# Performance work log

Hardware: AMD Instinct MI355X
Metric: run time of the kernel (lower is better)

## Reference

```python
import jax, jax.numpy as jnp
import numpy as np

B, S, T, H, V = 32, 64, 64, 512, 32000


def setup_inputs() -> dict:
    key = jax.random.key(0)
    ks = jax.random.split(key, 16)
    sc = 1.0 / np.sqrt(H)
    return {
        "encoder_outputs": jax.random.normal(ks[0], (B, S, H), jnp.float32),
        "encoder_hidden": jax.random.normal(ks[1], (1, B, H), jnp.float32),
        "target_tensor": jax.random.randint(ks[2], (B, T), 0, V),
        "max_len": T,
        "emb": jax.random.normal(ks[3], (V, H), jnp.float32) * 0.02,
        "Wa_w": jax.random.normal(ks[4], (H, H), jnp.float32) * sc,
        "Wa_b": jnp.zeros((H,), jnp.float32),
        "Ua_w": jax.random.normal(ks[5], (H, H), jnp.float32) * sc,
        "Ua_b": jnp.zeros((H,), jnp.float32),
        "Va_w": jax.random.normal(ks[6], (1, H), jnp.float32) * sc,
        "Va_b": jnp.zeros((1,), jnp.float32),
        "W_ih": jax.random.normal(ks[7], (3 * H, 2 * H), jnp.float32) * sc,
        "W_hh": jax.random.normal(ks[8], (3 * H, H), jnp.float32) * sc,
        "b_ih": jnp.zeros((3 * H,), jnp.float32),
        "b_hh": jnp.zeros((3 * H,), jnp.float32),
        "out_w": jax.random.normal(ks[9], (V, H), jnp.float32) * sc,
        "out_b": jnp.zeros((V,), jnp.float32),
    }


def reference(encoder_outputs, encoder_hidden, target_tensor, max_len,
              emb, Wa_w, Wa_b, Ua_w, Ua_b, Va_w, Va_b,
              W_ih, W_hh, b_ih, b_hh, out_w, out_b):
    # Teacher-forcing decode; dropout in eval mode (identity).
    keys = encoder_outputs                      # [B,S,H]
    Ua_keys = keys @ Ua_w.T + Ua_b              # precompute Ua(keys): same math each step
    bsz = keys.shape[0]
    # token fed at step 0 is SOS (=0), then target_tensor[:, i-1]
    tokens = jnp.concatenate(
        [jnp.zeros((bsz, 1), target_tensor.dtype), target_tensor[:, : max_len - 1]], axis=1
    )  # [B,T]

    def step(h, tok):                            # h: [B,H], tok: [B]
        e = emb[tok]                             # [B,H] embedding gather
        q = h @ Wa_w.T + Wa_b                    # Wa(query)
        s = jnp.tanh(q[:, None, :] + Ua_keys)    # [B,S,H]
        scores = (s @ Va_w.T + Va_b)[..., 0]     # [B,S]
        w = jax.nn.softmax(scores, axis=-1)      # [B,S]
        ctx = jnp.einsum('bs,bsh->bh', w, keys)  # [B,H]
        x = jnp.concatenate([e, ctx], axis=-1)   # [B,2H]
        gi = x @ W_ih.T + b_ih                   # [B,3H]
        gh = h @ W_hh.T + b_hh                   # [B,3H]
        ir, iz, inn = jnp.split(gi, 3, axis=-1)
        hr, hz, hn = jnp.split(gh, 3, axis=-1)
        r = jax.nn.sigmoid(ir + hr)
        z = jax.nn.sigmoid(iz + hz)
        n = jnp.tanh(inn + r * hn)
        h_new = (1.0 - z) * n + z * h            # GRU cell (PyTorch convention)
        logits = h_new @ out_w.T + out_b         # [B,V]
        return h_new, (logits, w)

    h0 = encoder_hidden[0]                       # [B,H]
    hT, (logits, attn) = jax.lax.scan(step, h0, jnp.swapaxes(tokens, 0, 1))
    logits = jnp.swapaxes(logits, 0, 1)          # [B,T,V]
    decoder_outputs = jax.nn.log_softmax(logits, axis=-1)
    attentions = jnp.swapaxes(attn, 0, 1)        # [B,T,S]
    return decoder_outputs, hT[None], attentions
```

## Files before the change

### kernel.cpp

```cpp
#include <hip/hip_runtime.h>
#include <hip/hip_bf16.h>
#include <hip/hip_fp16.h>
#include <math.h>

constexpr int B = 32, S = 64, T = 64, H = 512, V = 32000;
constexpr int G3 = 3 * H;
constexpr int BT = B * T;

constexpr size_t UAK_OFF    = 0;
constexpr size_t GIE_OFF    = 1048576;
constexpr size_t KWTH_OFF   = 4194304;
constexpr size_t WA2T_OFF   = 5767168;
constexpr size_t WHH2T_OFF  = 5898240;
constexpr size_t ROWIDX_OFF = 6291456;
constexpr size_t SCPT_OFF   = 6293504;
constexpr size_t FLG_OFF    = 7342080;
constexpr size_t OWBF_OFF   = 0;
constexpr size_t HALL_OFF   = 8192000;
constexpr size_t STATS_OFF  = 8192000;
constexpr size_t HBF_OFF    = 9256960;
constexpr size_t KEYSH_OFF  = 10000000;
constexpr size_t GEH_OFF    = 10524288;
constexpr size_t UAWH_OFF   = 11048576;
constexpr size_t WLOH_OFF   = 11179648;
constexpr size_t WCTXH_OFF  = 11572864;

typedef __attribute__((ext_vector_type(8))) short bf16x8;
typedef __attribute__((ext_vector_type(4))) float f32x4;
typedef _Float16 f16x8 __attribute__((ext_vector_type(8)));
typedef _Float16 h2v __attribute__((ext_vector_type(2)));

__device__ __forceinline__ float fast_tanh(float x) {
  float ax = fabsf(x);
  float e = __expf(-2.f * ax);
  float r = (1.f - e) / (1.f + e);
  return x < 0.f ? -r : r;
}
__device__ __forceinline__ float fast_sig(float x) {
  return 1.f / (1.f + __expf(-x));
}
__device__ __forceinline__ unsigned pack_h2(float a, float b) {
  __half2 h = __floats2half2_rn(a, b);
  return *(unsigned*)&h;
}
__device__ __forceinline__ ushort f2h(float v) {
  __half h = __float2half(v);
  return *(ushort*)&h;
}
__device__ __forceinline__ void unp2(unsigned v, float* d) {
  __half2 h = *(__half2*)&v;
  d[0] = __low2float(h); d[1] = __high2float(h);
}
__device__ __forceinline__ float dot2acc(unsigned w, unsigned h, float c) {
  return __builtin_amdgcn_fdot2(__builtin_bit_cast(h2v, w),
                                __builtin_bit_cast(h2v, h), c, false);
}
__device__ __forceinline__ int load_coh_i32(const int* p) {
  int v;
  asm volatile("global_load_dword %0, %1, off sc0 sc1\n\ts_waitcnt vmcnt(0)"
               : "=v"(v) : "v"(p) : "memory");
  return v;
}
__device__ __forceinline__ void store_coh_f32x4(float* p, f32x4 v) {
  asm volatile("global_store_dwordx4 %0, %1, off sc0 sc1" :: "v"(p), "v"(v) : "memory");
}

__global__ void k_init(const float* __restrict__ eh, const int* __restrict__ tgt,
                       float* __restrict__ ws) {
  int i = blockIdx.x * 256 + threadIdx.x;
  if (i < B * H) ws[HALL_OFF + i] = eh[i];
  if (i < BT) {
    int b = i / T, t = i % T;
    ((int*)(ws + ROWIDX_OFF))[i] = (t == 0) ? 0 : tgt[b * T + t - 1];
  }
  if (i < T * 64) ((int*)(ws + FLG_OFF))[i] = 0;
}

__global__ void k_conv_f16(const float* __restrict__ in, int ld, int coloff,
                           const int* __restrict__ rowidx, ushort* __restrict__ out,
                           int rows) {
  int i4 = (blockIdx.x * 256 + threadIdx.x) * 4;
  if (i4 < rows * 512) {
    int row = i4 >> 9, k = i4 & 511;
    int ar = rowidx ? rowidx[row] : row;
    float4 v = *(const float4*)&in[(size_t)ar * ld + coloff + k];
    ushort4 o;
    o.x = f2h(v.x); o.y = f2h(v.y); o.z = f2h(v.z); o.w = f2h(v.w);
    *(ushort4*)&out[i4] = o;
  }
}

__global__ void k_pack_t(const float* __restrict__ in, unsigned* __restrict__ out, int R) {
  int i = blockIdx.x * 256 + threadIdx.x;
  if (i < R * 256) {
    int r = i >> 8, kk = i & 255;
    float2 v = *(const float2*)&in[(size_t)r * 512 + 2 * kk];
    out[(size_t)kk * R + r] = pack_h2(v.x, v.y);
  }
}

__global__ void k_conv_outw(const float* __restrict__ w, ushort* __restrict__ o, int n4) {
  int i = blockIdx.x * blockDim.x + threadIdx.x;
  if (i < n4) {
    float4 v = *(const float4*)&w[(size_t)i * 4];
    ushort4 u;
    __hip_bfloat16 h0 = __float2bfloat16(v.x); u.x = *(ushort*)&h0;
    __hip_bfloat16 h1 = __float2bfloat16(v.y); u.y = *(ushort*)&h1;
    __hip_bfloat16 h2 = __float2bfloat16(v.z); u.z = *(ushort*)&h2;
    __hip_bfloat16 h3 = __float2bfloat16(v.w); u.w = *(ushort*)&h3;
    *(ushort4*)&o[(size_t)i * 4] = u;
  }
}

__global__ __launch_bounds__(256) void k_mfma128(
    const ushort* __restrict__ Ah, const ushort* __restrict__ Bh,
    const float* __restrict__ bias, float* __restrict__ C, int ldc) {
  __shared__ __align__(16) ushort As[128 * 32];
  __shared__ __align__(16) ushort Bs[128 * 32];
  int bm = blockIdx.y, bn = blockIdx.x;
  int tid = threadIdx.x;
  int lane = tid & 63, wv = tid >> 6;
  int wm = wv >> 1, wn = wv & 1;
  int kc = lane >> 4, rl = lane & 15;
  f32x4 acc[4][4] = {};
  int c0 = wv * 128 + lane, c1 = c0 + 64;
  const ushort* ga0 = Ah + (size_t)(bm * 128 + (c0 >> 2)) * 512 + (c0 & 3) * 8;
  const ushort* ga1 = Ah + (size_t)(bm * 128 + (c1 >> 2)) * 512 + (c1 & 3) * 8;
  const ushort* gb0 = Bh + (size_t)(bn * 128 + (c0 >> 2)) * 512 + (c0 & 3) * 8;
  const ushort* gb1 = Bh + (size_t)(bn * 128 + (c1 >> 2)) * 512 + (c1 & 3) * 8;
  for (int k0 = 0; k0 < 512; k0 += 32) {
    __syncthreads();
    __builtin_amdgcn_global_load_lds(
        (const __attribute__((address_space(1))) void*)(ga0 + k0),
        (__attribute__((address_space(3))) void*)((char*)As + wv * 2048), 16, 0, 0);
    __builtin_amdgcn_global_load_lds(
        (const __attribute__((address_space(1))) void*)(ga1 + k0),
        (__attribute__((address_space(3))) void*)((char*)As + wv * 2048 + 1024), 16, 0, 0);
    __builtin_amdgcn_global_load_lds(
        (const __attribute__((address_space(1))) void*)(gb0 + k0),
        (__attribute__((address_space(3))) void*)((char*)Bs + wv * 2048), 16, 0, 0);
    __builtin_amdgcn_global_load_lds(
        (const __attribute__((address_space(1))) void*)(gb1 + k0),
        (__attribute__((address_space(3))) void*)((char*)Bs + wv * 2048 + 1024), 16, 0, 0);
    __syncthreads();
    f16x8 af[4], bfv[4];
#pragma unroll
    for (int f = 0; f < 4; f++) {
      af[f] = *(const f16x8*)&As[(wm * 64 + f * 16 + rl) * 32 + kc * 8];
      bfv[f] = *(const f16x8*)&Bs[(wn * 64 + f * 16 + rl) * 32 + kc * 8];
    }
#pragma unroll
    for (int i = 0; i < 4; i++)
#pragma unroll
      for (int j = 0; j < 4; j++)
        acc[i][j] = __builtin_amdgcn_mfma_f32_16x16x32_f16(af[i], bfv[j], acc[i][j], 0, 0, 0);
  }
  int cl = lane & 15, rg = lane >> 4;
#pragma unroll
  for (int i = 0; i < 4; i++) {
    int m = bm * 128 + wm * 64 + i * 16 + rg * 4;
#pragma unroll
    for (int j = 0; j < 4; j++) {
      int n = bn * 128 + wn * 64 + j * 16 + cl;
      float bv = bias[n];
#pragma unroll
      for (int r = 0; r < 4; r++)
        C[(size_t)(m + r) * ldc + n] = acc[i][j][r] + bv;
    }
  }
}

__global__ __launch_bounds__(256) void k_mfma_kwt(
    const ushort* __restrict__ Wctxh, const ushort* __restrict__ keysh,
    ushort* __restrict__ KWTh) {
  __shared__ __align__(16) ushort As[128 * 32];
  __shared__ __align__(16) ushort Bs[64 * 32];
  int bm = blockIdx.x, b = blockIdx.y;
  int tid = threadIdx.x;
  int lane = tid & 63, wv = tid >> 6;
  int kc = lane >> 4, rl = lane & 15;
  f32x4 acc[2][4] = {};
  int c0 = tid, c2 = tid + 256;
  const ushort* ga0 = Wctxh + (size_t)(bm * 128 + (c0 >> 2)) * 512 + (c0 & 3) * 8;
  const ushort* ga1 = Wctxh + (size_t)(bm * 128 + (c2 >> 2)) * 512 + (c2 & 3) * 8;
  const ushort* gb0 = keysh + (size_t)(b * 64 + (c0 >> 2)) * 512 + (c0 & 3) * 8;
  for (int k0 = 0; k0 < 512; k0 += 32) {
    __syncthreads();
    __builtin_amdgcn_global_load_lds(
        (const __attribute__((address_space(1))) void*)(ga0 + k0),
        (__attribute__((address_space(3))) void*)((char*)As + wv * 1024), 16, 0, 0);
    __builtin_amdgcn_global_load_lds(
        (const __attribute__((address_space(1))) void*)(ga1 + k0),
        (__attribute__((address_space(3))) void*)((char*)As + 4096 + wv * 1024), 16, 0, 0);
    __builtin_amdgcn_global_load_lds(
        (const __attribute__((address_space(1))) void*)(gb0 + k0),
        (__attribute__((address_space(3))) void*)((char*)Bs + wv * 1024), 16, 0, 0);
    __syncthreads();
    f16x8 af[2], bfv[4];
#pragma unroll
    for (int f = 0; f < 2; f++)
      af[f] = *(const f16x8*)&As[(wv * 32 + f * 16 + rl) * 32 + kc * 8];
#pragma unroll
    for (int j = 0; j < 4; j++)
      bfv[j] = *(const f16x8*)&Bs[(j * 16 + rl) * 32 + kc * 8];
#pragma unroll
    for (int i = 0; i < 2; i++)
#pragma unroll
      for (int j = 0; j < 4; j++)
        acc[i][j] = __builtin_amdgcn_mfma_f32_16x16x32_f16(af[i], bfv[j], acc[i][j], 0, 0, 0);
  }
  int cl = lane & 15, rg = lane >> 4;
#pragma unroll
  for (int i = 0; i < 2; i++) {
    int m = bm * 128 + wv * 32 + i * 16 + rg * 4;
#pragma unroll
    for (int j = 0; j < 4; j++) {
      int n = j * 16 + cl;
#pragma unroll
      for (int r = 0; r < 4; r++)
        KWTh[((size_t)b * G3 + m + r) * 64 + n] = f2h(acc[i][j][r]);
    }
  }
}

__global__ __launch_bounds__(256) void k_recur(
    const float* __restrict__ Wa_b, const float* __restrict__ Va_w,
    const float* __restrict__ Va_b, const float* __restrict__ b_hh,
    const unsigned* __restrict__ WA2T, const unsigned* __restrict__ WHH2T,
    float* __restrict__ ws, float* __restrict__ attn_out) {
  const int w = blockIdx.x;
  const int tid = threadIdx.x;
  const int b = w & 31, cb = w >> 5;
  const int j0 = cb * 64;
  int* flg = (int*)(ws + FLG_OFF);
  __hip_bfloat16* HBF = (__hip_bfloat16*)(ws + HBF_OFF);
  const float* GIE = ws + GIE_OFF;
  float* SCPT = ws + SCPT_OFF;
  const ushort* KWTh = (const ushort*)(ws + KWTH_OFF);

  __shared__ float sKWT[192][68];
  __shared__ float sUAK[64][68];
  __shared__ float sh[512];
  __shared__ unsigned sH2[256];
  __shared__ float sq[64];
  __shared__ float qp[64][5];
  __shared__ float spp[64][5];
  __shared__ float sps[64];
  __shared__ float scg[8][64];
  __shared__ float swt[64];
  __shared__ float sga[4][64];
  __shared__ float shn[64];
  __shared__ float sVa[64], sWab[64], sBhh[192];

#pragma unroll
  for (int g = 0; g < 3; g++) {
    int jl = tid >> 2, part = tid & 3;
    const ushort* src = KWTh + ((size_t)b * G3 + g * 512 + j0 + jl) * 64 + part * 16;
    float* dst = &sKWT[g * 64 + jl][part * 16];
    uint4 u0 = *(const uint4*)src;
    uint4 u1 = *(const uint4*)(src + 8);
    unp2(u0.x, dst); unp2(u0.y, dst + 2); unp2(u0.z, dst + 4); unp2(u0.w, dst + 6);
    unp2(u1.x, dst + 8); unp2(u1.y, dst + 10); unp2(u1.z, dst + 12); unp2(u1.w, dst + 14);
  }
  {
    int s = tid >> 2, part = tid & 3;
    const float* src = ws + UAK_OFF + ((size_t)(b * 64 + s)) * 512 + j0 + part * 16;
    float* dst = &sUAK[s][part * 16];
#pragma unroll
    for (int i = 0; i < 16; i += 4) *(float4*)&dst[i] = *(const float4*)&src[i];
  }
  if (tid < 64) { sVa[tid] = Va_w[j0 + tid]; sWab[tid] = Wa_b[j0 + tid]; }
  if (tid < 192) sBhh[tid] = b_hh[(tid >> 6) * 512 + j0 + (tid & 63)];
  const float va_b = Va_b[0];
  __syncthreads();

  for (int t = 0; t < T; ++t) {
    if (t > 0) {
      if (tid == 0)
        while (load_coh_i32(&flg[(t - 1) * 64 + b * 2]) != 8) __builtin_amdgcn_s_sleep(1);
    }
    __syncthreads();
    const float* hcur = ws + HALL_OFF + (size_t)t * B * H + b * H;
    sh[tid] = hcur[tid];
    sh[tid + 256] = hcur[tid + 256];
    float gival = 0.f;
    if (tid < 192)
      gival = GIE[((size_t)b * T + t) * G3 + (tid >> 6) * 512 + j0 + (tid & 63)];
    __syncthreads();
    if (tid < 256) sH2[tid] = pack_h2(sh[2 * tid], sh[2 * tid + 1]);
    __syncthreads();

    {
      int jq = tid & 63, kp = tid >> 6;
      const unsigned* wp = WA2T + (size_t)(kp * 64) * 512 + j0 + jq;
      float acc = 0.f;
#pragma unroll 8
      for (int kk = 0; kk < 64; kk++)
        acc = dot2acc(wp[(size_t)kk * 512], sH2[kp * 64 + kk], acc);
      qp[jq][kp] = acc;
    }
    __syncthreads();
    if (tid < 64)
      sq[tid] = qp[tid][0] + qp[tid][1] + qp[tid][2] + qp[tid][3] + sWab[tid];
    __syncthreads();
    {
      int s = tid >> 2, jc = tid & 3;
      float accs = 0.f;
#pragma unroll
      for (int i = 0; i < 16; i++) {
        int j = jc * 16 + i;
        accs += sVa[j] * fast_tanh(sq[j] + sUAK[s][j]);
      }
      spp[s][jc] = accs;
    }
    __syncthreads();
    if (tid < 64) {
      float v = spp[tid][0] + spp[tid][1] + spp[tid][2] + spp[tid][3];
      if (cb == 0) v += va_b;
      sps[tid] = v;
    }
    __syncthreads();
    if (tid < 16)
      store_coh_f32x4(SCPT + (((size_t)t * B + b) * 8 + cb) * 64 + tid * 4,
                      *(f32x4*)&sps[tid * 4]);
    if (tid == 0) {
      asm volatile("s_waitcnt vmcnt(0)" ::: "memory");
      __hip_atomic_fetch_add(&flg[t * 64 + b * 2 + 1], 1,
                             __ATOMIC_RELAXED, __HIP_MEMORY_SCOPE_AGENT);
    }

    float gh = 0.f;
    if (tid < 192) {
      int gate = tid >> 6, lane = tid & 63;
      const unsigned* wp = WHH2T + gate * 512 + j0 + lane;
      float g0 = 0.f, g1 = 0.f;
#pragma unroll 8
      for (int kk = 0; kk < 256; kk += 2) {
        g0 = dot2acc(wp[(size_t)kk * 1536], sH2[kk], g0);
        g1 = dot2acc(wp[(size_t)(kk + 1) * 1536], sH2[kk + 1], g1);
      }
      gh = g0 + g1 + sBhh[tid];
    }
    if (tid == 0)
      while (load_coh_i32(&flg[t * 64 + b * 2 + 1]) != 8) __builtin_amdgcn_s_sleep(1);
    __syncthreads();
    if (tid < 128) {
      f32x4 v = *(const f32x4*)&SCPT[((size_t)t * B + b) * 512 + tid * 4];
      *(f32x4*)&scg[tid >> 4][(tid & 15) * 4] = v;
    }
    __syncthreads();
    if (tid < 64) {
      float v = scg[0][tid] + scg[1][tid] + scg[2][tid] + scg[3][tid]
              + scg[4][tid] + scg[5][tid] + scg[6][tid] + scg[7][tid];
      float m = v;
      for (int o = 32; o; o >>= 1) m = fmaxf(m, __shfl_xor(m, o, 64));
      float e = __expf(v - m);
      float su = e;
      for (int o = 32; o; o >>= 1) su += __shfl_xor(su, o, 64);
      float wt = e / su;
      swt[tid] = wt;
      if (cb == 0) attn_out[((size_t)b * T + t) * S + tid] = wt;
    }
    __syncthreads();
    if (tid < 192) {
      int gate = tid >> 6, lane = tid & 63;
      float gic = 0.f;
#pragma unroll
      for (int s4 = 0; s4 < 64; s4 += 4) {
        float4 k4 = *(const float4*)&sKWT[tid][s4];
        gic += k4.x * swt[s4] + k4.y * swt[s4 + 1] + k4.z * swt[s4 + 2] + k4.w * swt[s4 + 3];
      }
      float gi = gival + gic;
      if (gate == 0) sga[0][lane] = gi + gh;
      else if (gate == 1) sga[1][lane] = gi + gh;
      else { sga[2][lane] = gi; sga[3][lane] = gh; }
    }
    __syncthreads();
    if (tid < 64) {
      float r = fast_sig(sga[0][tid]);
      float z = fast_sig(sga[1][tid]);
      float n = fast_tanh(sga[2][tid] + r * sga[3][tid]);
      float hold = sh[j0 + tid];
      float hn = (1.f - z) * n + z * hold;
      shn[tid] = hn;
      HBF[((size_t)b * T + t) * H + j0 + tid] = __float2bfloat16(hn);
    }
    __syncthreads();
    if (tid < 16)
      store_coh_f32x4(ws + HALL_OFF + (size_t)(t + 1) * B * H + b * H + j0 + tid * 4,
                      *(f32x4*)&shn[tid * 4]);
    if (tid == 0) {
      asm volatile("s_waitcnt vmcnt(0)" ::: "memory");
      __hip_atomic_fetch_add(&flg[t * 64 + b * 2], 1,
                             __ATOMIC_RELAXED, __HIP_MEMORY_SCOPE_AGENT);
    }
  }
}

__global__ __launch_bounds__(256) void k_outgemm(
    const __hip_bfloat16* __restrict__ Abf, const __hip_bfloat16* __restrict__ Bbf,
    const float* __restrict__ bias, float* __restrict__ Cmat,
    float* __restrict__ stats) {
  __shared__ __align__(16) short As[128 * 32];
  __shared__ __align__(16) short Bs[128 * 32];
  __shared__ float sredM[2][128];
  __shared__ float sredS[2][128];
  int bm = blockIdx.y, bn = blockIdx.x;
  int tid = threadIdx.x;
  int lane = tid & 63, wv = tid >> 6;
  int wm = wv >> 1, wn = wv & 1;
  int kc = lane >> 4, rl = lane & 15;
  f32x4 acc[4][4] = {};
  int c0 = wv * 128 + lane, c1 = c0 + 64;
  const __hip_bfloat16* ga0 = Abf + (size_t)(bm * 128 + (c0 >> 2)) * 512 + (c0 & 3) * 8;
  const __hip_bfloat16* ga1 = Abf + (size_t)(bm * 128 + (c1 >> 2)) * 512 + (c1 & 3) * 8;
  const __hip_bfloat16* gb0 = Bbf + (size_t)(bn * 128 + (c0 >> 2)) * 512 + (c0 & 3) * 8;
  const __hip_bfloat16* gb1 = Bbf + (size_t)(bn * 128 + (c1 >> 2)) * 512 + (c1 & 3) * 8;
  for (int k0 = 0; k0 < 512; k0 += 32) {
    __syncthreads();
    __builtin_amdgcn_global_load_lds(
        (const __attribute__((address_space(1))) void*)(ga0 + k0),
        (__attribute__((address_space(3))) void*)((char*)As + wv * 2048), 16, 0, 0);
    __builtin_amdgcn_global_load_lds(
        (const __attribute__((address_space(1))) void*)(ga1 + k0),
        (__attribute__((address_space(3))) void*)((char*)As + wv * 2048 + 1024), 16, 0, 0);
    __builtin_amdgcn_global_load_lds(
        (const __attribute__((address_space(1))) void*)(gb0 + k0),
        (__attribute__((address_space(3))) void*)((char*)Bs + wv * 2048), 16, 0, 0);
    __builtin_amdgcn_global_load_lds(
        (const __attribute__((address_space(1))) void*)(gb1 + k0),
        (__attribute__((address_space(3))) void*)((char*)Bs + wv * 2048 + 1024), 16, 0, 0);
    __syncthreads();
    bf16x8 af[4], bfv[4];
#pragma unroll
    for (int f = 0; f < 4; f++) {
      af[f] = *(const bf16x8*)&As[(wm * 64 + f * 16 + rl) * 32 + kc * 8];
      bfv[f] = *(const bf16x8*)&Bs[(wn * 64 + f * 16 + rl) * 32 + kc * 8];
    }
#pragma unroll
    for (int i = 0; i < 4; i++)
#pragma unroll
      for (int j = 0; j < 4; j++)
        acc[i][j] = __builtin_amdgcn_mfma_f32_16x16x32_bf16(af[i], bfv[j], acc[i][j], 0, 0, 0);
  }
  int cl = lane & 15, rg = lane >> 4;
  float bv[4];
#pragma unroll
  for (int j = 0; j < 4; j++) bv[j] = bias[bn * 128 + wn * 64 + j * 16 + cl];
  float vmax[4][4];
#pragma unroll
  for (int i = 0; i < 4; i++) {
    int m = bm * 128 + wm * 64 + i * 16 + rg * 4;
#pragma unroll
    for (int r = 0; r < 4; r++) vmax[i][r] = -1e30f;
#pragma unroll
    for (int j = 0; j < 4; j++) {
      int n = bn * 128 + wn * 64 + j * 16 + cl;
#pragma unroll
      for (int r = 0; r < 4; r++) {
        float val = acc[i][j][r] + bv[j];
        Cmat[(size_t)(m + r) * V + n] = val;
        vmax[i][r] = fmaxf(vmax[i][r], val);
      }
    }
  }
#pragma unroll
  for (int o = 1; o < 16; o <<= 1)
#pragma unroll
    for (int i = 0; i < 4; i++)
#pragma unroll
      for (int r = 0; r < 4; r++)
        vmax[i][r] = fmaxf(vmax[i][r], __shfl_xor(vmax[i][r], o, 64));
  float vsum[4][4] = {};
#pragma unroll
  for (int i = 0; i < 4; i++)
#pragma unroll
    for (int j = 0; j < 4; j++)
#pragma unroll
      for (int r = 0; r < 4; r++)
        vsum[i][r] += __expf(acc[i][j][r] + bv[j] - vmax[i][r]);
#pragma unroll
  for (int o = 1; o < 16; o <<= 1)
#pragma unroll
    for (int i = 0; i < 4; i++)
#pragma unroll
      for (int r = 0; r < 4; r++)
        vsum[i][r] += __shfl_xor(vsum[i][r], o, 64);
  if (cl == 0) {
#pragma unroll
    for (int i = 0; i < 4; i++)
#pragma unroll
      for (int r = 0; r < 4; r++) {
        int rowl = wm * 64 + i * 16 + rg * 4 + r;
        sredM[wn][rowl] = vmax[i][r];
        sredS[wn][rowl] = vsum[i][r];
      }
  }
  __syncthreads();
  if (tid < 128) {
    float m0 = sredM[0][tid], m1 = sredM[1][tid];
    float M = fmaxf(m0, m1);
    float Sv = sredS[0][tid] * __expf(m0 - M) + sredS[1][tid] * __expf(m1 - M);
    float* st = stats + (size_t)(bm * 128 + tid) * 512 + bn * 2;
    st[0] = M; st[1] = Sv;
  }
}

__global__ __launch_bounds__(256) void k_lsm_final(float* __restrict__ Cmat,
                                                   const float* __restrict__ stats) {
  int row = blockIdx.x;
  int tid = threadIdx.x;
  __shared__ float sM[4], sS[4];
  float m = -1e30f, s = 0.f;
  if (tid < 250) {
    float2 v = *(const float2*)&stats[(size_t)row * 512 + tid * 2];
    m = v.x; s = v.y;
  }
  for (int o = 32; o; o >>= 1) {
    float om = __shfl_xor(m, o, 64), os = __shfl_xor(s, o, 64);
    float nm = fmaxf(m, om);
    s = s * __expf(m - nm) + os * __expf(om - nm);
    m = nm;
  }
  if ((tid & 63) == 0) { sM[tid >> 6] = m; sS[tid >> 6] = s; }
  __syncthreads();
  float M = fmaxf(fmaxf(sM[0], sM[1]), fmaxf(sM[2], sM[3]));
  float Ssum = sS[0] * __expf(sM[0] - M) + sS[1] * __expf(sM[1] - M)
             + sS[2] * __expf(sM[2] - M) + sS[3] * __expf(sM[3] - M);
  float lse = M + __logf(Ssum);
  float* p = Cmat + (size_t)row * V;
  for (int i = tid * 4; i < V; i += 1024) {
    float4 v = *(const float4*)&p[i];
    v.x -= lse; v.y -= lse; v.z -= lse; v.w -= lse;
    *(float4*)&p[i] = v;
  }
}

__global__ void k_copy_ht(const float* __restrict__ hsrc, float* __restrict__ o) {
  int i = blockIdx.x * 256 + threadIdx.x;
  if (i < B * H) o[i] = hsrc[i];
}

extern "C" void kernel_launch(void* const* d_in, const int* in_sizes, int n_in,
                              void* d_out, int out_size, void* d_ws, size_t ws_size,
                              hipStream_t stream) {
  (void)in_sizes; (void)n_in; (void)out_size; (void)ws_size;
  const float* keys = (const float*)d_in[0];
  const float* ehid = (const float*)d_in[1];
  const int* tgt    = (const int*)d_in[2];
  const float* emb  = (const float*)d_in[4];
  const float* Wa_w = (const float*)d_in[5];
  const float* Wa_b = (const float*)d_in[6];
  const float* Ua_w = (const float*)d_in[7];
  const float* Ua_b = (const float*)d_in[8];
  const float* Va_w = (const float*)d_in[9];
  const float* Va_b = (const float*)d_in[10];
  const float* W_ih = (const float*)d_in[11];
  const float* W_hh = (const float*)d_in[12];
  const float* b_ih = (const float*)d_in[13];
  const float* b_hh = (const float*)d_in[14];
  const float* out_w = (const float*)d_in[15];
  const float* out_b = (const float*)d_in[16];
  float* ws = (float*)d_ws;
  float* out = (float*)d_out;
  float* logits = out;
  float* ht_out = out + (size_t)B * T * V;
  float* attn_out = ht_out + (size_t)B * H;

  hipLaunchKernelGGL(k_init, dim3(64), dim3(256), 0, stream, ehid, tgt, ws);
  hipLaunchKernelGGL(k_conv_f16, dim3(1024), dim3(256), 0, stream,
                     keys, 512, 0, (const int*)nullptr, (ushort*)(ws + KEYSH_OFF), 2048);
  hipLaunchKernelGGL(k_conv_f16, dim3(1024), dim3(256), 0, stream,
                     emb, 512, 0, (const int*)(ws + ROWIDX_OFF), (ushort*)(ws + GEH_OFF), 2048);
  hipLaunchKernelGGL(k_conv_f16, dim3(256), dim3(256), 0, stream,
                     Ua_w, 512, 0, (const int*)nullptr, (ushort*)(ws + UAWH_OFF), 512);
  hipLaunchKernelGGL(k_conv_f16, dim3(768), dim3(256), 0, stream,
                     W_ih, 1024, 0, (const int*)nullptr, (ushort*)(ws + WLOH_OFF), 1536);
  hipLaunchKernelGGL(k_conv_f16, dim3(768), dim3(256), 0, stream,
                     W_ih, 1024, 512, (const int*)nullptr, (ushort*)(ws + WCTXH_OFF), 1536);
  hipLaunchKernelGGL(k_pack_t, dim3(512), dim3(256), 0, stream,
                     Wa_w, (unsigned*)(ws + WA2T_OFF), 512);
  hipLaunchKernelGGL(k_pack_t, dim3(1536), dim3(256), 0, stream,
                     W_hh, (unsigned*)(ws + WHH2T_OFF), 1536);
  hipLaunchKernelGGL(k_mfma128, dim3(4, 16), dim3(256), 0, stream,
                     (const ushort*)(ws + KEYSH_OFF), (const ushort*)(ws + UAWH_OFF),
                     Ua_b, ws + UAK_OFF, 512);
  hipLaunchKernelGGL(k_mfma128, dim3(12, 16), dim3(256), 0, stream,
                     (const ushort*)(ws + GEH_OFF), (const ushort*)(ws + WLOH_OFF),
                     b_ih, ws + GIE_OFF, G3);
  hipLaunchKernelGGL(k_mfma_kwt, dim3(12, 32), dim3(256), 0, stream,
                     (const ushort*)(ws + WCTXH_OFF), (const ushort*)(ws + KEYSH_OFF),
                     (ushort*)(ws + KWTH_OFF));
  hipLaunchKernelGGL(k_recur, dim3(256), dim3(256), 0, stream,
                     Wa_b, Va_w, Va_b, b_hh,
                     (const unsigned*)(ws + WA2T_OFF), (const unsigned*)(ws + WHH2T_OFF),
                     ws, attn_out);
  hipLaunchKernelGGL(k_copy_ht, dim3(64), dim3(256), 0, stream,
                     ws + HALL_OFF + (size_t)T * B * H, ht_out);
  hipLaunchKernelGGL(k_conv_outw, dim3((V * H / 4 + 255) / 256), dim3(256), 0, stream,
                     out_w, (ushort*)(ws + OWBF_OFF), V * H / 4);
  hipLaunchKernelGGL(k_outgemm, dim3(250, 16), dim3(256), 0, stream,
                     (const __hip_bfloat16*)(ws + HBF_OFF),
                     (const __hip_bfloat16*)(ws + OWBF_OFF), out_b, logits,
                     ws + STATS_OFF);
  hipLaunchKernelGGL(k_lsm_final, dim3(BT), dim3(256), 0, stream,
                     logits, ws + STATS_OFF);
}
```

Baseline: 1.013 ms.

## Replace atomic counters with per-block flag slots and merge prep kernels

Inter-block sync in the recurrent kernel now uses one flag slot per column block, polled with two coherent 16-byte loads, instead of atomic counters polled with sleeps. It also drops several shared-memory staging steps and barriers by storing h and score partials directly with coherent scalar stores. Eight small preprocessing launches become one multi-role k_prep kernel, and the final hidden state is written inside the recurrence, removing the copy kernel. This targets per-step sync latency and launch overhead, at the cost of more flag memory and busy-spinning without sleep.

```diff
diff --git a/kernel.cpp b/kernel.cpp
--- a/kernel.cpp
+++ b/kernel.cpp
@@ -12,9 +12,8 @@
 constexpr size_t KWTH_OFF   = 4194304;
 constexpr size_t WA2T_OFF   = 5767168;
 constexpr size_t WHH2T_OFF  = 5898240;
-constexpr size_t ROWIDX_OFF = 6291456;
-constexpr size_t SCPT_OFF   = 6293504;
-constexpr size_t FLG_OFF    = 7342080;
+constexpr size_t SCPT_OFF   = 6291456;
+constexpr size_t FLG_OFF    = 7340032;
 constexpr size_t OWBF_OFF   = 0;
 constexpr size_t HALL_OFF   = 8192000;
 constexpr size_t STATS_OFF  = 8192000;
@@ -27,6 +26,7 @@
 
 typedef __attribute__((ext_vector_type(8))) short bf16x8;
 typedef __attribute__((ext_vector_type(4))) float f32x4;
+typedef __attribute__((ext_vector_type(4))) int i32x4;
 typedef _Float16 f16x8 __attribute__((ext_vector_type(8)));
 typedef _Float16 h2v __attribute__((ext_vector_type(2)));
 
@@ -55,47 +55,84 @@
   return __builtin_amdgcn_fdot2(__builtin_bit_cast(h2v, w),
                                 __builtin_bit_cast(h2v, h), c, false);
 }
-__device__ __forceinline__ int load_coh_i32(const int* p) {
-  int v;
-  asm volatile("global_load_dword %0, %1, off sc0 sc1\n\ts_waitcnt vmcnt(0)"
-               : "=v"(v) : "v"(p) : "memory");
-  return v;
-}
-__device__ __forceinline__ void store_coh_f32x4(float* p, f32x4 v) {
-  asm volatile("global_store_dwordx4 %0, %1, off sc0 sc1" :: "v"(p), "v"(v) : "memory");
-}
-
-__global__ void k_init(const float* __restrict__ eh, const int* __restrict__ tgt,
+__device__ __forceinline__ int poll8(const int* p) {
+  i32x4 a, b;
+  asm volatile("global_load_dwordx4 %0, %2, off sc0 sc1\n\t"
+               "global_load_dwordx4 %1, %3, off sc0 sc1\n\t"
+               "s_waitcnt vmcnt(0)"
+               : "=v"(a), "=v"(b) : "v"(p), "v"(p + 4) : "memory");
+  return a.x & a.y & a.z & a.w & b.x & b.y & b.z & b.w;
+}
+__device__ __forceinline__ void store_coh_i32(int* p, int v) {
+  asm volatile("global_store_dword %0, %1, off sc0 sc1" :: "v"(p), "v"(v) : "memory");
+}
+__device__ __forceinline__ void store_coh_f32(float* p, float v) {
+  asm volatile("global_store_dword %0, %1, off sc0 sc1" :: "v"(p), "v"(v) : "memory");
+}
+
+__global__ void k_prep(const float* __restrict__ eh, const int* __restrict__ tgt,
+                       const float* __restrict__ keys, const float* __restrict__ emb,
+                       const float* __restrict__ Ua_w, const float* __restrict__ W_ih,
+                       const float* __restrict__ Wa_w, const float* __restrict__ W_hh,
                        float* __restrict__ ws) {
-  int i = blockIdx.x * 256 + threadIdx.x;
-  if (i < B * H) ws[HALL_OFF + i] = eh[i];
-  if (i < BT) {
-    int b = i / T, t = i % T;
-    ((int*)(ws + ROWIDX_OFF))[i] = (t == 0) ? 0 : tgt[b * T + t - 1];
-  }
-  if (i < T * 64) ((int*)(ws + FLG_OFF))[i] = 0;
-}
-
-__global__ void k_conv_f16(const float* __restrict__ in, int ld, int coloff,
-                           const int* __restrict__ rowidx, ushort* __restrict__ out,
-                           int rows) {
-  int i4 = (blockIdx.x * 256 + threadIdx.x) * 4;
-  if (i4 < rows * 512) {
+  int blk = blockIdx.x, tid = threadIdx.x;
+  if (blk < 256) {
+    int i = blk * 256 + tid;
+    ((int*)(ws + FLG_OFF))[i] = 0;
+    if (i < B * H) ws[HALL_OFF + i] = eh[i];
+    return;
+  }
+  if (blk < 1280) {
+    int i4 = ((blk - 256) * 256 + tid) * 4;
+    float4 v = *(const float4*)&keys[i4];
+    ushort4 o; o.x = f2h(v.x); o.y = f2h(v.y); o.z = f2h(v.z); o.w = f2h(v.w);
+    *(ushort4*)&((ushort*)(ws + KEYSH_OFF))[i4] = o;
+    return;
+  }
+  if (blk < 2304) {
+    int i4 = ((blk - 1280) * 256 + tid) * 4;
     int row = i4 >> 9, k = i4 & 511;
-    int ar = rowidx ? rowidx[row] : row;
-    float4 v = *(const float4*)&in[(size_t)ar * ld + coloff + k];
-    ushort4 o;
-    o.x = f2h(v.x); o.y = f2h(v.y); o.z = f2h(v.z); o.w = f2h(v.w);
-    *(ushort4*)&out[i4] = o;
-  }
-}
-
-__global__ void k_pack_t(const float* __restrict__ in, unsigned* __restrict__ out, int R) {
-  int i = blockIdx.x * 256 + threadIdx.x;
-  if (i < R * 256) {
+    int tok = (row & 63) ? tgt[row - 1] : 0;
+    float4 v = *(const float4*)&emb[(size_t)tok * 512 + k];
+    ushort4 o; o.x = f2h(v.x); o.y = f2h(v.y); o.z = f2h(v.z); o.w = f2h(v.w);
+    *(ushort4*)&((ushort*)(ws + GEH_OFF))[i4] = o;
+    return;
+  }
+  if (blk < 2560) {
+    int i4 = ((blk - 2304) * 256 + tid) * 4;
+    float4 v = *(const float4*)&Ua_w[i4];
+    ushort4 o; o.x = f2h(v.x); o.y = f2h(v.y); o.z = f2h(v.z); o.w = f2h(v.w);
+    *(ushort4*)&((ushort*)(ws + UAWH_OFF))[i4] = o;
+    return;
+  }
+  if (blk < 3328) {
+    int i4 = ((blk - 2560) * 256 + tid) * 4;
+    int row = i4 >> 9, k = i4 & 511;
+    float4 v = *(const float4*)&W_ih[(size_t)row * 1024 + k];
+    ushort4 o; o.x = f2h(v.x); o.y = f2h(v.y); o.z = f2h(v.z); o.w = f2h(v.w);
+    *(ushort4*)&((ushort*)(ws + WLOH_OFF))[i4] = o;
+    return;
+  }
+  if (blk < 4096) {
+    int i4 = ((blk - 3328) * 256 + tid) * 4;
+    int row = i4 >> 9, k = i4 & 511;
+    float4 v = *(const float4*)&W_ih[(size_t)row * 1024 + 512 + k];
+    ushort4 o; o.x = f2h(v.x); o.y = f2h(v.y); o.z = f2h(v.z); o.w = f2h(v.w);
+    *(ushort4*)&((ushort*)(ws + WCTXH_OFF))[i4] = o;
+    return;
+  }
+  if (blk < 4608) {
+    int i = (blk - 4096) * 256 + tid;
     int r = i >> 8, kk = i & 255;
-    float2 v = *(const float2*)&in[(size_t)r * 512 + 2 * kk];
-    out[(size_t)kk * R + r] = pack_h2(v.x, v.y);
+    float2 v = *(const float2*)&Wa_w[(size_t)r * 512 + 2 * kk];
+    ((unsigned*)(ws + WA2T_OFF))[(size_t)kk * 512 + r] = pack_h2(v.x, v.y);
+    return;
+  }
+  {
+    int i = (blk - 4608) * 256 + tid;
+    int r = i >> 8, kk = i & 255;
+    float2 v = *(const float2*)&W_hh[(size_t)r * 512 + 2 * kk];
+    ((unsigned*)(ws + WHH2T_OFF))[(size_t)kk * 1536 + r] = pack_h2(v.x, v.y);
   }
 }
 
@@ -227,7 +264,7 @@
     const float* __restrict__ Wa_b, const float* __restrict__ Va_w,
     const float* __restrict__ Va_b, const float* __restrict__ b_hh,
     const unsigned* __restrict__ WA2T, const unsigned* __restrict__ WHH2T,
-    float* __restrict__ ws, float* __restrict__ attn_out) {
+    float* __restrict__ ws, float* __restrict__ attn_out, float* __restrict__ ht_out) {
   const int w = blockIdx.x;
   const int tid = threadIdx.x;
   const int b = w & 31, cb = w >> 5;
@@ -240,16 +277,12 @@
 
   __shared__ float sKWT[192][68];
   __shared__ float sUAK[64][68];
-  __shared__ float sh[512];
   __shared__ unsigned sH2[256];
   __shared__ float sq[64];
   __shared__ float qp[64][5];
   __shared__ float spp[64][5];
-  __shared__ float sps[64];
-  __shared__ float scg[8][64];
   __shared__ float swt[64];
   __shared__ float sga[4][64];
-  __shared__ float shn[64];
   __shared__ float sVa[64], sWab[64], sBhh[192];
 
 #pragma unroll
@@ -275,19 +308,21 @@
   __syncthreads();
 
   for (int t = 0; t < T; ++t) {
-    if (t > 0) {
-      if (tid == 0)
-        while (load_coh_i32(&flg[(t - 1) * 64 + b * 2]) != 8) __builtin_amdgcn_s_sleep(1);
-    }
-    __syncthreads();
     const float* hcur = ws + HALL_OFF + (size_t)t * B * H + b * H;
-    sh[tid] = hcur[tid];
-    sh[tid + 256] = hcur[tid + 256];
     float gival = 0.f;
     if (tid < 192)
       gival = GIE[((size_t)b * T + t) * G3 + (tid >> 6) * 512 + j0 + (tid & 63)];
-    __syncthreads();
-    if (tid < 256) sH2[tid] = pack_h2(sh[2 * tid], sh[2 * tid + 1]);
+    if (t > 0) {
+      if (tid == 0) {
+        const int* fb = flg + (size_t)(t - 1) * 1024 + b * 32;
+        while (!poll8(fb)) {}
+      }
+    }
+    __syncthreads();
+    {
+      float2 h2 = *(const float2*)&hcur[2 * tid];
+      sH2[tid] = pack_h2(h2.x, h2.y);
+    }
     __syncthreads();
 
     {
@@ -317,16 +352,11 @@
     if (tid < 64) {
       float v = spp[tid][0] + spp[tid][1] + spp[tid][2] + spp[tid][3];
       if (cb == 0) v += va_b;
-      sps[tid] = v;
-    }
-    __syncthreads();
-    if (tid < 16)
-      store_coh_f32x4(SCPT + (((size_t)t * B + b) * 8 + cb) * 64 + tid * 4,
-                      *(f32x4*)&sps[tid * 4]);
+      store_coh_f32(SCPT + (((size_t)t * B + b) * 8 + cb) * 64 + tid, v);
+    }
     if (tid == 0) {
       asm volatile("s_waitcnt vmcnt(0)" ::: "memory");
-      __hip_atomic_fetch_add(&flg[t * 64 + b * 2 + 1], 1,
-                             __ATOMIC_RELAXED, __HIP_MEMORY_SCOPE_AGENT);
+      store_coh_i32(flg + (size_t)t * 1024 + b * 32 + 8 + cb, 1);
     }
 
     float gh = 0.f;
@@ -341,17 +371,15 @@
       }
       gh = g0 + g1 + sBhh[tid];
     }
-    if (tid == 0)
-      while (load_coh_i32(&flg[t * 64 + b * 2 + 1]) != 8) __builtin_amdgcn_s_sleep(1);
-    __syncthreads();
-    if (tid < 128) {
-      f32x4 v = *(const f32x4*)&SCPT[((size_t)t * B + b) * 512 + tid * 4];
-      *(f32x4*)&scg[tid >> 4][(tid & 15) * 4] = v;
+    if (tid == 0) {
+      const int* fs = flg + (size_t)t * 1024 + b * 32 + 8;
+      while (!poll8(fs)) {}
     }
     __syncthreads();
     if (tid < 64) {
-      float v = scg[0][tid] + scg[1][tid] + scg[2][tid] + scg[3][tid]
-              + scg[4][tid] + scg[5][tid] + scg[6][tid] + scg[7][tid];
+      const float* sp = SCPT + ((size_t)t * B + b) * 512;
+      float v = (sp[tid] + sp[64 + tid]) + (sp[128 + tid] + sp[192 + tid])
+              + (sp[256 + tid] + sp[320 + tid]) + (sp[384 + tid] + sp[448 + tid]);
       float m = v;
       for (int o = 32; o; o >>= 1) m = fmaxf(m, __shfl_xor(m, o, 64));
       float e = __expf(v - m);
@@ -380,20 +408,19 @@
       float r = fast_sig(sga[0][tid]);
       float z = fast_sig(sga[1][tid]);
       float n = fast_tanh(sga[2][tid] + r * sga[3][tid]);
-      float hold = sh[j0 + tid];
+      float hold = hcur[j0 + tid];
       float hn = (1.f - z) * n + z * hold;
-      shn[tid] = hn;
       HBF[((size_t)b * T + t) * H + j0 + tid] = __float2bfloat16(hn);
-    }
-    __syncthreads();
-    if (tid < 16)
-      store_coh_f32x4(ws + HALL_OFF + (size_t)(t + 1) * B * H + b * H + j0 + tid * 4,
-                      *(f32x4*)&shn[tid * 4]);
-    if (tid == 0) {
+      if (t < T - 1)
+        store_coh_f32(ws + HALL_OFF + (size_t)(t + 1) * B * H + b * H + j0 + tid, hn);
+      else
+        ht_out[b * H + j0 + tid] = hn;
+    }
+    if (tid == 0 && t < T - 1) {
       asm volatile("s_waitcnt vmcnt(0)" ::: "memory");
-      __hip_atomic_fetch_add(&flg[t * 64 + b * 2], 1,
-                             __ATOMIC_RELAXED, __HIP_MEMORY_SCOPE_AGENT);
-    }
+      store_coh_i32(flg + (size_t)t * 1024 + b * 32 + cb, 1);
+    }
+    __syncthreads();
   }
 }
 
@@ -534,11 +561,6 @@
     v.x -= lse; v.y -= lse; v.z -= lse; v.w -= lse;
     *(float4*)&p[i] = v;
   }
-}
-
-__global__ void k_copy_ht(const float* __restrict__ hsrc, float* __restrict__ o) {
-  int i = blockIdx.x * 256 + threadIdx.x;
-  if (i < B * H) o[i] = hsrc[i];
 }
 
 extern "C" void kernel_launch(void* const* d_in, const int* in_sizes, int n_in,
@@ -567,21 +589,8 @@
   float* ht_out = out + (size_t)B * T * V;
   float* attn_out = ht_out + (size_t)B * H;
 
-  hipLaunchKernelGGL(k_init, dim3(64), dim3(256), 0, stream, ehid, tgt, ws);
-  hipLaunchKernelGGL(k_conv_f16, dim3(1024), dim3(256), 0, stream,
-                     keys, 512, 0, (const int*)nullptr, (ushort*)(ws + KEYSH_OFF), 2048);
-  hipLaunchKernelGGL(k_conv_f16, dim3(1024), dim3(256), 0, stream,
-                     emb, 512, 0, (const int*)(ws + ROWIDX_OFF), (ushort*)(ws + GEH_OFF), 2048);
-  hipLaunchKernelGGL(k_conv_f16, dim3(256), dim3(256), 0, stream,
-                     Ua_w, 512, 0, (const int*)nullptr, (ushort*)(ws + UAWH_OFF), 512);
-  hipLaunchKernelGGL(k_conv_f16, dim3(768), dim3(256), 0, stream,
-                     W_ih, 1024, 0, (const int*)nullptr, (ushort*)(ws + WLOH_OFF), 1536);
-  hipLaunchKernelGGL(k_conv_f16, dim3(768), dim3(256), 0, stream,
-                     W_ih, 1024, 512, (const int*)nullptr, (ushort*)(ws + WCTXH_OFF), 1536);
-  hipLaunchKernelGGL(k_pack_t, dim3(512), dim3(256), 0, stream,
-                     Wa_w, (unsigned*)(ws + WA2T_OFF), 512);
-  hipLaunchKernelGGL(k_pack_t, dim3(1536), dim3(256), 0, stream,
-                     W_hh, (unsigned*)(ws + WHH2T_OFF), 1536);
+  hipLaunchKernelGGL(k_prep, dim3(6144), dim3(256), 0, stream,
+                     ehid, tgt, keys, emb, Ua_w, W_ih, Wa_w, W_hh, ws);
   hipLaunchKernelGGL(k_mfma128, dim3(4, 16), dim3(256), 0, stream,
                      (const ushort*)(ws + KEYSH_OFF), (const ushort*)(ws + UAWH_OFF),
                      Ua_b, ws + UAK_OFF, 512);
@@ -594,9 +603,7 @@
   hipLaunchKernelGGL(k_recur, dim3(256), dim3(256), 0, stream,
                      Wa_b, Va_w, Va_b, b_hh,
                      (const unsigned*)(ws + WA2T_OFF), (const unsigned*)(ws + WHH2T_OFF),
-                     ws, attn_out);
-  hipLaunchKernelGGL(k_copy_ht, dim3(64), dim3(256), 0, stream,
-                     ws + HALL_OFF + (size_t)T * B * H, ht_out);
+                     ws, attn_out, ht_out);
   hipLaunchKernelGGL(k_conv_outw, dim3((V * H / 4 + 255) / 256), dim3(256), 0, stream,
                      out_w, (ushort*)(ws + OWBF_OFF), V * H / 4);
   hipLaunchKernelGGL(k_outgemm, dim3(250, 16), dim3(256), 0, stream,
```

New measurement: 956.4 us. -5.6%, faster.
